# Performance work log

Measured on AMD Instinct MI355X. Metric: run time of the kernel, lower is better.

Reference implementation:

```python
import jax, jax.numpy as jnp
import numpy as np

N = 1_000_000   # total nodes
B = 20_000      # number of graphs (segments)
V = 100_000     # item vocab (rows of feat table)
D = 128         # input_dim
H = 128         # hidden_dim
O = 256         # output_dim
EPS = 1e-5


def setup_inputs() -> dict:
    key = jax.random.key(0)
    ks = jax.random.split(key, 10)
    feat = jax.random.normal(ks[0], (V, D), dtype=jnp.float32)
    iid = jax.random.randint(ks[1], (N,), 0, V)
    segment_ids = jnp.sort(jax.random.randint(ks[2], (N,), 0, B))
    last_nodes = jax.random.randint(ks[3], (B,), 0, N)
    s = 1.0 / np.sqrt(D)
    gamma = jnp.ones((D,), jnp.float32)
    beta = jnp.zeros((D,), jnp.float32)
    W_u = jax.random.uniform(ks[4], (D, H), jnp.float32, -s, s)
    W_v = jax.random.uniform(ks[5], (D, H), jnp.float32, -s, s)
    b_v = jax.random.uniform(ks[6], (H,), jnp.float32, -s, s)
    w_e = jax.random.uniform(ks[7], (H,), jnp.float32, -1.0 / np.sqrt(H), 1.0 / np.sqrt(H))
    W_out = jax.random.uniform(ks[8], (D, O), jnp.float32, -s, s)
    return {"feat": feat, "iid": iid, "segment_ids": segment_ids,
            "last_nodes": last_nodes, "gamma": gamma, "beta": beta,
            "W_u": W_u, "W_v": W_v, "b_v": b_v, "w_e": w_e, "W_out": W_out}


def reference(feat, iid, segment_ids, last_nodes, gamma, beta, W_u, W_v, b_v, w_e, W_out):
    # gather per-node features from item table
    x = feat[iid]                                  # [N, D]
    # BatchNorm1d (training mode: batch statistics, biased var)
    mean = jnp.mean(x, axis=0)
    var = jnp.mean((x - mean) ** 2, axis=0)
    x = (x - mean) * jax.lax.rsqrt(var + EPS) * gamma + beta
    # projections
    feat_u = x @ W_u                               # [N, H]
    feat_v = x[last_nodes] @ W_v + b_v             # [B, H]
    e = jax.nn.sigmoid(feat_u + feat_v[segment_ids]) @ w_e   # [N]
    # segment softmax over per-graph node segments
    e_max = jax.ops.segment_max(e, segment_ids, num_segments=B)
    ex = jnp.exp(e - e_max[segment_ids])
    denom = jax.ops.segment_sum(ex, segment_ids, num_segments=B)
    alpha = ex / denom[segment_ids]                # [N]
    # weighted segment sum, then output projection
    rst = jax.ops.segment_sum(x * alpha[:, None], segment_ids, num_segments=B)  # [B, D]
    return rst @ W_out                             # [B, O]
```

## Files before the change

### kernel.cpp

```cpp
#include <hip/hip_runtime.h>

typedef __attribute__((ext_vector_type(8))) short short8;
typedef __attribute__((ext_vector_type(4))) float floatx4;
typedef __attribute__((ext_vector_type(4))) int intx4;

static __device__ __forceinline__ unsigned short f2bf(float x) {
    unsigned int u = __float_as_uint(x);
    u += 0x7fffu + ((u >> 16) & 1u);
    return (unsigned short)(u >> 16);
}

template <int CTRL>
static __device__ __forceinline__ float dpp_add(float x) {
    int v = __builtin_amdgcn_update_dpp(0, __float_as_int(x), CTRL, 0xf, 0xf, true);
    return x + __int_as_float(v);
}

__global__ void k_hist(const int* __restrict__ iid, int* __restrict__ counts, int N) {
    int n = blockIdx.x * blockDim.x + threadIdx.x;
    if (n < N) atomicAdd(&counts[iid[n]], 1);
}

__global__ __launch_bounds__(256) void k_cvtstats(const float* __restrict__ feat,
                                                  const int* __restrict__ counts,
                                                  unsigned short* __restrict__ featb,
                                                  float* __restrict__ dsum, float* __restrict__ dsumsq,
                                                  int V) {
    int tid = threadIdx.x;
    int r2 = tid >> 7, d = tid & 127;
    float s = 0.f, qa = 0.f;
    for (int vp = blockIdx.x; vp * 2 < V; vp += gridDim.x) {
        int v = vp * 2 + r2;
        if (v >= V) continue;
        float f = feat[(size_t)v * 128 + d];
        featb[(size_t)v * 128 + d] = f2bf(f);
        float c = (float)counts[v];
        if (c != 0.f) { s += c * f; qa += c * f * f; }
    }
    __shared__ float red[256];
    red[tid] = s; __syncthreads();
    if (tid < 128) atomicAdd(&dsum[d], red[tid] + red[tid + 128]);
    __syncthreads();
    red[tid] = qa; __syncthreads();
    if (tid < 128) atomicAdd(&dsumsq[d], red[tid] + red[tid + 128]);
}

__global__ __launch_bounds__(128) void k_affine(const float* __restrict__ sum,
                                                const float* __restrict__ sumsq,
                                                const float* __restrict__ gamma,
                                                const float* __restrict__ beta,
                                                float* __restrict__ scale, float* __restrict__ shift,
                                                float invN) {
    int d = threadIdx.x;
    float mean = sum[d] * invN;
    float var  = sumsq[d] * invN - mean * mean;
    float sc   = gamma[d] * rsqrtf(var + 1e-5f);
    scale[d] = sc;
    shift[d] = beta[d] - mean * sc;
}

__global__ __launch_bounds__(128) void k_prep(const float* __restrict__ Wu, const float* __restrict__ Wv,
                                              const float* __restrict__ bv,
                                              const float* __restrict__ scale, const float* __restrict__ shift,
                                              unsigned short* __restrict__ wut, float* __restrict__ wvs,
                                              float* __restrict__ cbias) {
    int h = blockIdx.x, d = threadIdx.x;
    float sc = scale[d], sh = shift[d];
    float wu = Wu[d * 128 + h], wv = Wv[d * 128 + h];
    wut[h * 128 + d] = f2bf(sc * wu);
    wvs[d * 128 + h] = sc * wv;
    __shared__ float red[128];
    red[d] = sh * (wu + wv);
    __syncthreads();
    for (int off = 64; off > 0; off >>= 1) {
        if (d < off) red[d] += red[d + off];
        __syncthreads();
    }
    if (d == 0) cbias[h] = bv[h] + red[0];
}

__global__ __launch_bounds__(128) void k_fv(const float* __restrict__ feat, const int* __restrict__ iid,
                                            const int* __restrict__ last, const float* __restrict__ wvs,
                                            const float* __restrict__ cbias, float* __restrict__ fv,
                                            int B) {
    const int GPB = 8;
    int b0 = blockIdx.x * GPB;
    int h = threadIdx.x;
    __shared__ float sx[GPB][128];
    for (int g = 0; g < GPB; ++g) {
        int b = b0 + g;
        if (b < B) {
            int row = iid[last[b]];
            sx[g][h] = feat[(size_t)row * 128 + h];
        }
    }
    __syncthreads();
    float acc[GPB];
#pragma unroll
    for (int g = 0; g < GPB; ++g) acc[g] = 0.f;
    for (int d = 0; d < 128; ++d) {
        float w = wvs[d * 128 + h];
#pragma unroll
        for (int g = 0; g < GPB; ++g) acc[g] += sx[g][d] * w;
    }
    float c = cbias[h];
    for (int g = 0; g < GPB; ++g)
        if (b0 + g < B) fv[(size_t)(b0 + g) * 128 + h] = acc[g] + c;
}

__global__ __launch_bounds__(256, 4) void k_main(
        const unsigned short* __restrict__ featb, const int* __restrict__ iid,
        const int* __restrict__ seg, const unsigned short* __restrict__ wut,
        const float* __restrict__ fv, const float* __restrict__ we_g,
        float* __restrict__ rstAcc, float* __restrict__ den,
        int N, int B, int numTiles) {
    __shared__ unsigned short sA[2][64 * 128];
    __shared__ int   sSeg[2][64];
    __shared__ float sFv[2][4][128];
    __shared__ float sEp[4][64];

    int tid = threadIdx.x;
    int wv = tid >> 6, lane = tid & 63, q = lane >> 4, c = lane & 15;
    int p2 = lane & 15;

    short8 bfr[2][4];
    float we2[2];
#pragma unroll
    for (int t = 0; t < 2; ++t) {
        int h = (2 * wv + t) * 16 + c;
        we2[t] = we_g[h];
#pragma unroll
        for (int kc = 0; kc < 4; ++kc)
            bfr[t][kc] = *(const short8*)(wut + h * 128 + kc * 32 + q * 8);
    }

    if (blockIdx.x >= numTiles) return;

    int iidR[4]; int segR; float2 fvR;
    int rowbase = wv * 16 + (lane >> 4);
    auto loadRegs = [&](int T) {
        int n0 = T << 6;
#pragma unroll
        for (int k = 0; k < 4; ++k)
            iidR[k] = iid[min(n0 + rowbase + 4 * k, N - 1)];
        segR = seg[min(n0 + (tid & 63), N - 1)];
        int s0 = seg[min(n0, N - 1)];
        int fvrow = min(s0 + (tid >> 6), B - 1);
        fvR = *(const float2*)(fv + (size_t)fvrow * 128 + ((tid << 1) & 127));
    };
    auto stage = [&](int buf) {
        unsigned short* sAb = &sA[buf][0];
#pragma unroll
        for (int k = 0; k < 4; ++k) {
            int row = rowbase + 4 * k;
            int j = (p2 & 8) | ((p2 & 7) ^ (row & 7));
            const unsigned short* g = featb + (size_t)iidR[k] * 128 + j * 8;
            __builtin_amdgcn_global_load_lds(
                (const __attribute__((address_space(1))) void*)g,
                (__attribute__((address_space(3))) void*)(sAb + wv * 2048 + k * 512),
                16, 0, 0);
        }
        if (tid < 64) sSeg[buf][tid] = segR;
        *(float2*)&sFv[buf][tid >> 6][(tid << 1) & 127] = fvR;
    };

    int T = blockIdx.x;
    loadRegs(T);
    stage(0);
    int cur = 0;

    for (;;) {
        int Tn = T + gridDim.x;
        bool hn = (Tn < numTiles);
        if (hn) loadRegs(Tn);
        __syncthreads();
        if (hn) stage(cur ^ 1);

        floatx4 acc[4][2];
#pragma unroll
        for (int mt = 0; mt < 4; ++mt)
#pragma unroll
            for (int t = 0; t < 2; ++t) acc[mt][t] = (floatx4)(0.f);
#pragma unroll
        for (int kc = 0; kc < 4; ++kc) {
            int jj = 4 * kc + q;
            int pofs = ((jj & 8) | ((jj & 7) ^ (c & 7))) * 8;
            short8 a0 = *(const short8*)&sA[cur][( 0 + c) * 128 + pofs];
            short8 a1 = *(const short8*)&sA[cur][(16 + c) * 128 + pofs];
            short8 a2 = *(const short8*)&sA[cur][(32 + c) * 128 + pofs];
            short8 a3 = *(const short8*)&sA[cur][(48 + c) * 128 + pofs];
#pragma unroll
            for (int t = 0; t < 2; ++t) {
                acc[0][t] = __builtin_amdgcn_mfma_f32_16x16x32_bf16(a0, bfr[t][kc], acc[0][t], 0, 0, 0);
                acc[1][t] = __builtin_amdgcn_mfma_f32_16x16x32_bf16(a1, bfr[t][kc], acc[1][t], 0, 0, 0);
                acc[2][t] = __builtin_amdgcn_mfma_f32_16x16x32_bf16(a2, bfr[t][kc], acc[2][t], 0, 0, 0);
                acc[3][t] = __builtin_amdgcn_mfma_f32_16x16x32_bf16(a3, bfr[t][kc], acc[3][t], 0, 0, 0);
            }
        }
        {
            int s0 = sSeg[cur][0];
            int h0 = wv * 32 + c;
#pragma unroll
            for (int mt = 0; mt < 4; ++mt)
#pragma unroll
                for (int r = 0; r < 4; ++r) {
                    int nl = mt * 16 + q * 4 + r;
                    int sg = sSeg[cur][nl];
                    int off = sg - s0;
                    float f0, f1;
                    if (off < 4) {
                        f0 = sFv[cur][off][h0];
                        f1 = sFv[cur][off][h0 + 16];
                    } else {
                        f0 = fv[((size_t)sg << 7) + h0];
                        f1 = fv[((size_t)sg << 7) + h0 + 16];
                    }
                    float u0 = acc[mt][0][r] + f0;
                    float u1 = acc[mt][1][r] + f1;
                    float p = we2[0] * __builtin_amdgcn_rcpf(1.f + __expf(-u0))
                            + we2[1] * __builtin_amdgcn_rcpf(1.f + __expf(-u1));
                    p = dpp_add<0xb1>(p);
                    p = dpp_add<0x4e>(p);
                    p = dpp_add<0x141>(p);
                    p = dpp_add<0x140>(p);
                    if (c == 0) sEp[wv][nl] = p;
                }
        }
        asm volatile("s_waitcnt lgkmcnt(0)" ::: "memory");
        __builtin_amdgcn_s_barrier();
        __builtin_amdgcn_sched_barrier(0);

        {
            int n0 = T << 6;
            int nb = wv * 16;
            float exr[16];
#pragma unroll
            for (int jg = 0; jg < 4; ++jg) {
                floatx4 e0 = *(const floatx4*)&sEp[0][nb + jg * 4];
                floatx4 e1 = *(const floatx4*)&sEp[1][nb + jg * 4];
                floatx4 e2 = *(const floatx4*)&sEp[2][nb + jg * 4];
                floatx4 e3 = *(const floatx4*)&sEp[3][nb + jg * 4];
#pragma unroll
                for (int r = 0; r < 4; ++r) {
                    float s = e0[r] + e1[r] + e2[r] + e3[r];
                    exr[jg * 4 + r] = (n0 + nb + jg * 4 + r < N) ? __expf(s) : 0.f;
                }
            }
            int sgr[16];
#pragma unroll
            for (int jg = 0; jg < 4; ++jg)
                *(intx4*)&sgr[jg * 4] = *(const intx4*)&sSeg[cur][nb + jg * 4];

            int d0 = lane * 2;
            int jj = lane >> 2;
            int wsub = (lane & 3) * 4;
            const char* base = (const char*)&sA[cur][0];
            float a0 = 0.f, a1 = 0.f, dl = 0.f;
            int curseg = sgr[0];
#pragma unroll
            for (int j = 0; j < 16; ++j) {
                int row = nb + j;
                int sg = sgr[j];
                if (sg != curseg) {
                    atomicAdd(&rstAcc[(size_t)curseg * 128 + d0], a0);
                    atomicAdd(&rstAcc[(size_t)curseg * 128 + d0 + 1], a1);
                    if (lane == 0) atomicAdd(&den[curseg], dl);
                    a0 = a1 = dl = 0.f; curseg = sg;
                }
                int ch = (jj & 8) | ((jj & 7) ^ (row & 7));
                unsigned u = *(const unsigned*)(base + row * 256 + ch * 16 + wsub);
                float e = exr[j];
                a0 += e * __uint_as_float(u << 16);
                a1 += e * __uint_as_float(u & 0xffff0000u);
                dl += e;
            }
            atomicAdd(&rstAcc[(size_t)curseg * 128 + d0], a0);
            atomicAdd(&rstAcc[(size_t)curseg * 128 + d0 + 1], a1);
            if (lane == 0) atomicAdd(&den[curseg], dl);
        }

        if (!hn) break;
        T = Tn; cur ^= 1;
    }
}

__global__ __launch_bounds__(256) void k_out(const float* __restrict__ rstAcc,
                                             const float* __restrict__ den,
                                             const float* __restrict__ scale,
                                             const float* __restrict__ shift,
                                             const float* __restrict__ Wout,
                                             float* __restrict__ out, int B) {
    __shared__ float sT[128][36];
    __shared__ float sInv[32];
    int b0 = blockIdx.x * 32;
    int t = threadIdx.x;
    for (int i = 0; i < 16; ++i) {
        int idx = i * 256 + t;
        int r = idx >> 7, d = idx & 127;
        int b = min(b0 + r, B - 1);
        sT[d][r] = scale[d] * rstAcc[((size_t)b << 7) + d];
    }
    if (t < 32) {
        int b = min(b0 + t, B - 1);
        float dn = den[b];
        sInv[t] = (dn > 0.f) ? 1.f / dn : 0.f;
    }
    __syncthreads();
    float acc[32];
#pragma unroll
    for (int r = 0; r < 32; ++r) acc[r] = 0.f;
    float sb = 0.f;
    for (int dd = 0; dd < 128; ++dd) {
        float w = Wout[dd * 256 + t];
        sb += shift[dd] * w;
        const float4* row = (const float4*)&sT[dd][0];
#pragma unroll
        for (int r4 = 0; r4 < 8; ++r4) {
            float4 v = row[r4];
            acc[r4 * 4 + 0] += w * v.x;
            acc[r4 * 4 + 1] += w * v.y;
            acc[r4 * 4 + 2] += w * v.z;
            acc[r4 * 4 + 3] += w * v.w;
        }
    }
    for (int r = 0; r < 32; ++r)
        if (b0 + r < B) {
            float inv = sInv[r];
            out[(size_t)(b0 + r) * 256 + t] = acc[r] * inv + (inv != 0.f ? sb : 0.f);
        }
}

extern "C" void kernel_launch(void* const* d_in, const int* in_sizes, int n_in,
                              void* d_out, int out_size, void* d_ws, size_t ws_size,
                              hipStream_t stream) {
    const float* feat  = (const float*)d_in[0];
    const int*   iid   = (const int*)d_in[1];
    const int*   seg   = (const int*)d_in[2];
    const int*   last  = (const int*)d_in[3];
    const float* gamma = (const float*)d_in[4];
    const float* beta  = (const float*)d_in[5];
    const float* Wu    = (const float*)d_in[6];
    const float* Wv    = (const float*)d_in[7];
    const float* bv    = (const float*)d_in[8];
    const float* we    = (const float*)d_in[9];
    const float* Wout  = (const float*)d_in[10];
    float* out = (float*)d_out;

    int V = in_sizes[0] / 128;
    int N = in_sizes[1];
    int B = in_sizes[3];

    char* w = (char*)d_ws;
    size_t off = 0;
    auto alloc = [&](size_t bytes) -> void* {
        void* p = w + off;
        off += (bytes + 255) & ~(size_t)255;
        return p;
    };
    int*   counts = (int*)alloc((size_t)V * 4);
    float* dsum   = (float*)alloc(512);
    float* dsumsq = (float*)alloc(512);
    float* rstAcc = (float*)alloc((size_t)B * 128 * 4);
    float* den    = (float*)alloc((size_t)B * 4);
    size_t zero_bytes = off;
    float* scale  = (float*)alloc(512);
    float* shift  = (float*)alloc(512);
    float* cbias  = (float*)alloc(512);
    unsigned short* wut = (unsigned short*)alloc(128 * 128 * 2);
    float* wvs    = (float*)alloc(128 * 128 * 4);
    float* fv     = (float*)alloc((size_t)B * 128 * 4);
    unsigned short* featb = (unsigned short*)alloc((size_t)V * 128 * 2);
    (void)ws_size; (void)n_in; (void)out_size;

    hipMemsetAsync(d_ws, 0, zero_bytes, stream);

    k_hist<<<(N + 255) / 256, 256, 0, stream>>>(iid, counts, N);
    k_cvtstats<<<1024, 256, 0, stream>>>(feat, counts, featb, dsum, dsumsq, V);
    k_affine<<<1, 128, 0, stream>>>(dsum, dsumsq, gamma, beta, scale, shift, 1.0f / (float)N);
    k_prep<<<128, 128, 0, stream>>>(Wu, Wv, bv, scale, shift, wut, wvs, cbias);
    k_fv<<<(B + 7) / 8, 128, 0, stream>>>(feat, iid, last, wvs, cbias, fv, B);

    int numTiles = (N + 63) / 64;
    k_main<<<1024, 256, 0, stream>>>(featb, iid, seg, wut, fv, we, rstAcc, den, N, B, numTiles);

    k_out<<<(B + 31) / 32, 256, 0, stream>>>(rstAcc, den, scale, shift, Wout, out, B);
}
```

Baseline: 416.3 us.

## Merge all stages into one cooperative persistent kernel with grid syncs

Replaces the memset and seven separate kernel launches with one cooperative kernel that runs each stage in sequence, separated by grid-wide barriers. Zeroing is done in-kernel and the small stages (affine, prep, fv, output projection) become grid-stride loops inside the same grid. The aim is to remove launch gaps and per-kernel ramp-up and tail costs. In exchange, the small serial stages run inside a 1024-block grid where most blocks sit idle at barriers, grid.sync adds its own overhead, and occupancy is now capped by the shared-memory and register use of the largest stage.

New measurement: 960.1 us. 2.31x slower.

```diff
diff --git a/kernel.cpp b/kernel.cpp
--- a/kernel.cpp
+++ b/kernel.cpp
@@ -1,4 +1,7 @@
 #include <hip/hip_runtime.h>
+#include <hip/hip_cooperative_groups.h>
+
+namespace cg = cooperative_groups;
 
 typedef __attribute__((ext_vector_type(8))) short short8;
 typedef __attribute__((ext_vector_type(4))) float floatx4;
@@ -16,335 +19,347 @@
     return x + __int_as_float(v);
 }
 
-__global__ void k_hist(const int* __restrict__ iid, int* __restrict__ counts, int N) {
-    int n = blockIdx.x * blockDim.x + threadIdx.x;
-    if (n < N) atomicAdd(&counts[iid[n]], 1);
-}
-
-__global__ __launch_bounds__(256) void k_cvtstats(const float* __restrict__ feat,
-                                                  const int* __restrict__ counts,
-                                                  unsigned short* __restrict__ featb,
-                                                  float* __restrict__ dsum, float* __restrict__ dsumsq,
-                                                  int V) {
+struct MonoP {
+    const float* feat; const int* iid; const int* seg; const int* last;
+    const float* gamma; const float* beta; const float* Wu; const float* Wv;
+    const float* bv; const float* we; const float* Wout;
+    float* out;
+    int* counts; float* dsum; float* dsumsq; float* rstAcc; float* den;
+    float* scale; float* shift; float* cbias;
+    unsigned short* wut; float* wvs; float* fv;
+    unsigned short* featb;
+    float* zeroBase; int zeroQuads;
+    int N, B, V, numTiles;
+};
+
+__global__ __launch_bounds__(256, 4) void k_mono(MonoP p) {
+    cg::grid_group grid = cg::this_grid();
+    __shared__ __align__(16) char smem[38912];
     int tid = threadIdx.x;
-    int r2 = tid >> 7, d = tid & 127;
-    float s = 0.f, qa = 0.f;
-    for (int vp = blockIdx.x; vp * 2 < V; vp += gridDim.x) {
-        int v = vp * 2 + r2;
-        if (v >= V) continue;
-        float f = feat[(size_t)v * 128 + d];
-        featb[(size_t)v * 128 + d] = f2bf(f);
-        float c = (float)counts[v];
-        if (c != 0.f) { s += c * f; qa += c * f * f; }
-    }
-    __shared__ float red[256];
-    red[tid] = s; __syncthreads();
-    if (tid < 128) atomicAdd(&dsum[d], red[tid] + red[tid + 128]);
-    __syncthreads();
-    red[tid] = qa; __syncthreads();
-    if (tid < 128) atomicAdd(&dsumsq[d], red[tid] + red[tid + 128]);
-}
-
-__global__ __launch_bounds__(128) void k_affine(const float* __restrict__ sum,
-                                                const float* __restrict__ sumsq,
-                                                const float* __restrict__ gamma,
-                                                const float* __restrict__ beta,
-                                                float* __restrict__ scale, float* __restrict__ shift,
-                                                float invN) {
-    int d = threadIdx.x;
-    float mean = sum[d] * invN;
-    float var  = sumsq[d] * invN - mean * mean;
-    float sc   = gamma[d] * rsqrtf(var + 1e-5f);
-    scale[d] = sc;
-    shift[d] = beta[d] - mean * sc;
-}
-
-__global__ __launch_bounds__(128) void k_prep(const float* __restrict__ Wu, const float* __restrict__ Wv,
-                                              const float* __restrict__ bv,
-                                              const float* __restrict__ scale, const float* __restrict__ shift,
-                                              unsigned short* __restrict__ wut, float* __restrict__ wvs,
-                                              float* __restrict__ cbias) {
-    int h = blockIdx.x, d = threadIdx.x;
-    float sc = scale[d], sh = shift[d];
-    float wu = Wu[d * 128 + h], wv = Wv[d * 128 + h];
-    wut[h * 128 + d] = f2bf(sc * wu);
-    wvs[d * 128 + h] = sc * wv;
-    __shared__ float red[128];
-    red[d] = sh * (wu + wv);
-    __syncthreads();
-    for (int off = 64; off > 0; off >>= 1) {
-        if (d < off) red[d] += red[d + off];
+    int gtid = blockIdx.x * 256 + tid;
+    int gsz = gridDim.x * 256;
+
+    {
+        floatx4* z = (floatx4*)p.zeroBase;
+        floatx4 zz = (floatx4)(0.f);
+        for (int i = gtid; i < p.zeroQuads; i += gsz) z[i] = zz;
+    }
+    grid.sync();
+
+    for (int n = gtid; n < p.N; n += gsz) atomicAdd(&p.counts[p.iid[n]], 1);
+    grid.sync();
+
+    {
+        float* red = (float*)smem;
+        int r2 = tid >> 7, d = tid & 127;
+        float s = 0.f, qa = 0.f;
+        for (int vp = blockIdx.x; vp * 2 < p.V; vp += gridDim.x) {
+            int v = vp * 2 + r2;
+            if (v >= p.V) continue;
+            float f = p.feat[(size_t)v * 128 + d];
+            p.featb[(size_t)v * 128 + d] = f2bf(f);
+            float c = (float)p.counts[v];
+            if (c != 0.f) { s += c * f; qa += c * f * f; }
+        }
+        red[tid] = s; __syncthreads();
+        if (tid < 128) atomicAdd(&p.dsum[d], red[tid] + red[tid + 128]);
         __syncthreads();
-    }
-    if (d == 0) cbias[h] = bv[h] + red[0];
-}
-
-__global__ __launch_bounds__(128) void k_fv(const float* __restrict__ feat, const int* __restrict__ iid,
-                                            const int* __restrict__ last, const float* __restrict__ wvs,
-                                            const float* __restrict__ cbias, float* __restrict__ fv,
-                                            int B) {
-    const int GPB = 8;
-    int b0 = blockIdx.x * GPB;
-    int h = threadIdx.x;
-    __shared__ float sx[GPB][128];
-    for (int g = 0; g < GPB; ++g) {
-        int b = b0 + g;
-        if (b < B) {
-            int row = iid[last[b]];
-            sx[g][h] = feat[(size_t)row * 128 + h];
-        }
-    }
-    __syncthreads();
-    float acc[GPB];
-#pragma unroll
-    for (int g = 0; g < GPB; ++g) acc[g] = 0.f;
-    for (int d = 0; d < 128; ++d) {
-        float w = wvs[d * 128 + h];
-#pragma unroll
-        for (int g = 0; g < GPB; ++g) acc[g] += sx[g][d] * w;
-    }
-    float c = cbias[h];
-    for (int g = 0; g < GPB; ++g)
-        if (b0 + g < B) fv[(size_t)(b0 + g) * 128 + h] = acc[g] + c;
-}
-
-__global__ __launch_bounds__(256, 4) void k_main(
-        const unsigned short* __restrict__ featb, const int* __restrict__ iid,
-        const int* __restrict__ seg, const unsigned short* __restrict__ wut,
-        const float* __restrict__ fv, const float* __restrict__ we_g,
-        float* __restrict__ rstAcc, float* __restrict__ den,
-        int N, int B, int numTiles) {
-    __shared__ unsigned short sA[2][64 * 128];
-    __shared__ int   sSeg[2][64];
-    __shared__ float sFv[2][4][128];
-    __shared__ float sEp[4][64];
-
-    int tid = threadIdx.x;
-    int wv = tid >> 6, lane = tid & 63, q = lane >> 4, c = lane & 15;
-    int p2 = lane & 15;
-
-    short8 bfr[2][4];
-    float we2[2];
-#pragma unroll
-    for (int t = 0; t < 2; ++t) {
-        int h = (2 * wv + t) * 16 + c;
-        we2[t] = we_g[h];
-#pragma unroll
-        for (int kc = 0; kc < 4; ++kc)
-            bfr[t][kc] = *(const short8*)(wut + h * 128 + kc * 32 + q * 8);
-    }
-
-    if (blockIdx.x >= numTiles) return;
-
-    int iidR[4]; int segR; float2 fvR;
-    int rowbase = wv * 16 + (lane >> 4);
-    auto loadRegs = [&](int T) {
-        int n0 = T << 6;
-#pragma unroll
-        for (int k = 0; k < 4; ++k)
-            iidR[k] = iid[min(n0 + rowbase + 4 * k, N - 1)];
-        segR = seg[min(n0 + (tid & 63), N - 1)];
-        int s0 = seg[min(n0, N - 1)];
-        int fvrow = min(s0 + (tid >> 6), B - 1);
-        fvR = *(const float2*)(fv + (size_t)fvrow * 128 + ((tid << 1) & 127));
-    };
-    auto stage = [&](int buf) {
-        unsigned short* sAb = &sA[buf][0];
-#pragma unroll
-        for (int k = 0; k < 4; ++k) {
-            int row = rowbase + 4 * k;
-            int j = (p2 & 8) | ((p2 & 7) ^ (row & 7));
-            const unsigned short* g = featb + (size_t)iidR[k] * 128 + j * 8;
-            __builtin_amdgcn_global_load_lds(
-                (const __attribute__((address_space(1))) void*)g,
-                (__attribute__((address_space(3))) void*)(sAb + wv * 2048 + k * 512),
-                16, 0, 0);
-        }
-        if (tid < 64) sSeg[buf][tid] = segR;
-        *(float2*)&sFv[buf][tid >> 6][(tid << 1) & 127] = fvR;
-    };
-
-    int T = blockIdx.x;
-    loadRegs(T);
-    stage(0);
-    int cur = 0;
-
-    for (;;) {
-        int Tn = T + gridDim.x;
-        bool hn = (Tn < numTiles);
-        if (hn) loadRegs(Tn);
+        red[tid] = qa; __syncthreads();
+        if (tid < 128) atomicAdd(&p.dsumsq[d], red[tid] + red[tid + 128]);
+    }
+    grid.sync();
+
+    if (blockIdx.x == 0 && tid < 128) {
+        int d = tid;
+        float invN = 1.f / (float)p.N;
+        float mean = p.dsum[d] * invN;
+        float var  = p.dsumsq[d] * invN - mean * mean;
+        float sc   = p.gamma[d] * rsqrtf(var + 1e-5f);
+        p.scale[d] = sc;
+        p.shift[d] = p.beta[d] - mean * sc;
+    }
+    grid.sync();
+
+    if (blockIdx.x < 64) {
+        float (*red)[128] = (float(*)[128])smem;
+        int d = tid & 127, half = tid >> 7;
+        int h = blockIdx.x * 2 + half;
+        float sc = p.scale[d], sh = p.shift[d];
+        float wu = p.Wu[d * 128 + h], wvv = p.Wv[d * 128 + h];
+        p.wut[h * 128 + d] = f2bf(sc * wu);
+        p.wvs[d * 128 + h] = sc * wvv;
+        red[half][d] = sh * (wu + wvv);
         __syncthreads();
-        if (hn) stage(cur ^ 1);
-
-        floatx4 acc[4][2];
-#pragma unroll
-        for (int mt = 0; mt < 4; ++mt)
-#pragma unroll
-            for (int t = 0; t < 2; ++t) acc[mt][t] = (floatx4)(0.f);
-#pragma unroll
-        for (int kc = 0; kc < 4; ++kc) {
-            int jj = 4 * kc + q;
-            int pofs = ((jj & 8) | ((jj & 7) ^ (c & 7))) * 8;
-            short8 a0 = *(const short8*)&sA[cur][( 0 + c) * 128 + pofs];
-            short8 a1 = *(const short8*)&sA[cur][(16 + c) * 128 + pofs];
-            short8 a2 = *(const short8*)&sA[cur][(32 + c) * 128 + pofs];
-            short8 a3 = *(const short8*)&sA[cur][(48 + c) * 128 + pofs];
-#pragma unroll
-            for (int t = 0; t < 2; ++t) {
-                acc[0][t] = __builtin_amdgcn_mfma_f32_16x16x32_bf16(a0, bfr[t][kc], acc[0][t], 0, 0, 0);
-                acc[1][t] = __builtin_amdgcn_mfma_f32_16x16x32_bf16(a1, bfr[t][kc], acc[1][t], 0, 0, 0);
-                acc[2][t] = __builtin_amdgcn_mfma_f32_16x16x32_bf16(a2, bfr[t][kc], acc[2][t], 0, 0, 0);
-                acc[3][t] = __builtin_amdgcn_mfma_f32_16x16x32_bf16(a3, bfr[t][kc], acc[3][t], 0, 0, 0);
-            }
-        }
-        {
-            int s0 = sSeg[cur][0];
-            int h0 = wv * 32 + c;
+        for (int off = 64; off > 0; off >>= 1) {
+            if (d < off) red[half][d] += red[half][d + off];
+            __syncthreads();
+        }
+        if (d == 0) p.cbias[h] = p.bv[h] + red[half][0];
+    }
+    grid.sync();
+
+    {
+        float (*sx)[128] = (float(*)[128])smem;
+        int h = tid & 127, half = tid >> 7;
+        int njob = (p.B + 15) >> 4;
+        for (int job = blockIdx.x; job < njob; job += gridDim.x) {
+            __syncthreads();
+            for (int g = 0; g < 8; ++g) {
+                int b = job * 16 + half * 8 + g;
+                if (b < p.B) {
+                    int row = p.iid[p.last[b]];
+                    sx[half * 8 + g][h] = p.feat[(size_t)row * 128 + h];
+                }
+            }
+            __syncthreads();
+            float acc[8];
+#pragma unroll
+            for (int g = 0; g < 8; ++g) acc[g] = 0.f;
+            for (int d = 0; d < 128; ++d) {
+                float w = p.wvs[d * 128 + h];
+#pragma unroll
+                for (int g = 0; g < 8; ++g) acc[g] += sx[half * 8 + g][d] * w;
+            }
+            float cb = p.cbias[h];
+            for (int g = 0; g < 8; ++g) {
+                int b = job * 16 + half * 8 + g;
+                if (b < p.B) p.fv[(size_t)b * 128 + h] = acc[g] + cb;
+            }
+        }
+    }
+    grid.sync();
+
+    if (blockIdx.x < p.numTiles) {
+        auto sA   = (unsigned short(*)[64 * 128])(smem);
+        auto sSeg = (int(*)[64])(smem + 32768);
+        auto sFv  = (float(*)[4][128])(smem + 33280);
+        auto sEp  = (float(*)[64])(smem + 37376);
+
+        int wv = tid >> 6, lane = tid & 63, q = lane >> 4, c = lane & 15;
+        int p2 = lane & 15;
+
+        short8 bfr[2][4];
+        float we2[2];
+#pragma unroll
+        for (int t = 0; t < 2; ++t) {
+            int h = (2 * wv + t) * 16 + c;
+            we2[t] = p.we[h];
+#pragma unroll
+            for (int kc = 0; kc < 4; ++kc)
+                bfr[t][kc] = *(const short8*)(p.wut + h * 128 + kc * 32 + q * 8);
+        }
+
+        int iidR[4]; int segR; float2 fvR;
+        int rowbase = wv * 16 + (lane >> 4);
+        auto loadRegs = [&](int T) {
+            int n0 = T << 6;
+#pragma unroll
+            for (int k = 0; k < 4; ++k)
+                iidR[k] = p.iid[min(n0 + rowbase + 4 * k, p.N - 1)];
+            segR = p.seg[min(n0 + (tid & 63), p.N - 1)];
+            int s0 = p.seg[min(n0, p.N - 1)];
+            int fvrow = min(s0 + (tid >> 6), p.B - 1);
+            fvR = *(const float2*)(p.fv + (size_t)fvrow * 128 + ((tid << 1) & 127));
+        };
+        auto stage = [&](int buf) {
+            unsigned short* sAb = &sA[buf][0];
+#pragma unroll
+            for (int k = 0; k < 4; ++k) {
+                int row = rowbase + 4 * k;
+                int j = (p2 & 8) | ((p2 & 7) ^ (row & 7));
+                const unsigned short* g = p.featb + (size_t)iidR[k] * 128 + j * 8;
+                __builtin_amdgcn_global_load_lds(
+                    (const __attribute__((address_space(1))) void*)g,
+                    (__attribute__((address_space(3))) void*)(sAb + wv * 2048 + k * 512),
+                    16, 0, 0);
+            }
+            if (tid < 64) sSeg[buf][tid] = segR;
+            *(float2*)&sFv[buf][tid >> 6][(tid << 1) & 127] = fvR;
+        };
+
+        int T = blockIdx.x;
+        loadRegs(T);
+        stage(0);
+        int cur = 0;
+
+        for (;;) {
+            int Tn = T + gridDim.x;
+            bool hn = (Tn < p.numTiles);
+            if (hn) loadRegs(Tn);
+            __syncthreads();
+            if (hn) stage(cur ^ 1);
+
+            floatx4 acc[4][2];
 #pragma unroll
             for (int mt = 0; mt < 4; ++mt)
 #pragma unroll
-                for (int r = 0; r < 4; ++r) {
-                    int nl = mt * 16 + q * 4 + r;
-                    int sg = sSeg[cur][nl];
-                    int off = sg - s0;
-                    float f0, f1;
-                    if (off < 4) {
-                        f0 = sFv[cur][off][h0];
-                        f1 = sFv[cur][off][h0 + 16];
-                    } else {
-                        f0 = fv[((size_t)sg << 7) + h0];
-                        f1 = fv[((size_t)sg << 7) + h0 + 16];
+                for (int t = 0; t < 2; ++t) acc[mt][t] = (floatx4)(0.f);
+#pragma unroll
+            for (int kc = 0; kc < 4; ++kc) {
+                int jj = 4 * kc + q;
+                int pofs = ((jj & 8) | ((jj & 7) ^ (c & 7))) * 8;
+                short8 a0 = *(const short8*)&sA[cur][( 0 + c) * 128 + pofs];
+                short8 a1 = *(const short8*)&sA[cur][(16 + c) * 128 + pofs];
+                short8 a2 = *(const short8*)&sA[cur][(32 + c) * 128 + pofs];
+                short8 a3 = *(const short8*)&sA[cur][(48 + c) * 128 + pofs];
+#pragma unroll
+                for (int t = 0; t < 2; ++t) {
+                    acc[0][t] = __builtin_amdgcn_mfma_f32_16x16x32_bf16(a0, bfr[t][kc], acc[0][t], 0, 0, 0);
+                    acc[1][t] = __builtin_amdgcn_mfma_f32_16x16x32_bf16(a1, bfr[t][kc], acc[1][t], 0, 0, 0);
+                    acc[2][t] = __builtin_amdgcn_mfma_f32_16x16x32_bf16(a2, bfr[t][kc], acc[2][t], 0, 0, 0);
+                    acc[3][t] = __builtin_amdgcn_mfma_f32_16x16x32_bf16(a3, bfr[t][kc], acc[3][t], 0, 0, 0);
+                }
+            }
+            {
+                int s0 = sSeg[cur][0];
+                int h0 = wv * 32 + c;
+#pragma unroll
+                for (int mt = 0; mt < 4; ++mt)
+#pragma unroll
+                    for (int r = 0; r < 4; ++r) {
+                        int nl = mt * 16 + q * 4 + r;
+                        int sg = sSeg[cur][nl];
+                        int off = sg - s0;
+                        float f0, f1;
+                        if (off < 4) {
+                            f0 = sFv[cur][off][h0];
+                            f1 = sFv[cur][off][h0 + 16];
+                        } else {
+                            f0 = p.fv[((size_t)sg << 7) + h0];
+                            f1 = p.fv[((size_t)sg << 7) + h0 + 16];
+                        }
+                        float u0 = acc[mt][0][r] + f0;
+                        float u1 = acc[mt][1][r] + f1;
+                        float pp = we2[0] * __builtin_amdgcn_rcpf(1.f + __expf(-u0))
+                                 + we2[1] * __builtin_amdgcn_rcpf(1.f + __expf(-u1));
+                        pp = dpp_add<0xb1>(pp);
+                        pp = dpp_add<0x4e>(pp);
+                        pp = dpp_add<0x141>(pp);
+                        pp = dpp_add<0x140>(pp);
+                        if (c == 0) sEp[wv][nl] = pp;
                     }
-                    float u0 = acc[mt][0][r] + f0;
-                    float u1 = acc[mt][1][r] + f1;
-                    float p = we2[0] * __builtin_amdgcn_rcpf(1.f + __expf(-u0))
-                            + we2[1] * __builtin_amdgcn_rcpf(1.f + __expf(-u1));
-                    p = dpp_add<0xb1>(p);
-                    p = dpp_add<0x4e>(p);
-                    p = dpp_add<0x141>(p);
-                    p = dpp_add<0x140>(p);
-                    if (c == 0) sEp[wv][nl] = p;
-                }
-        }
-        asm volatile("s_waitcnt lgkmcnt(0)" ::: "memory");
-        __builtin_amdgcn_s_barrier();
-        __builtin_amdgcn_sched_barrier(0);
-
-        {
-            int n0 = T << 6;
-            int nb = wv * 16;
-            float exr[16];
-#pragma unroll
-            for (int jg = 0; jg < 4; ++jg) {
-                floatx4 e0 = *(const floatx4*)&sEp[0][nb + jg * 4];
-                floatx4 e1 = *(const floatx4*)&sEp[1][nb + jg * 4];
-                floatx4 e2 = *(const floatx4*)&sEp[2][nb + jg * 4];
-                floatx4 e3 = *(const floatx4*)&sEp[3][nb + jg * 4];
-#pragma unroll
-                for (int r = 0; r < 4; ++r) {
-                    float s = e0[r] + e1[r] + e2[r] + e3[r];
-                    exr[jg * 4 + r] = (n0 + nb + jg * 4 + r < N) ? __expf(s) : 0.f;
-                }
-            }
-            int sgr[16];
-#pragma unroll
-            for (int jg = 0; jg < 4; ++jg)
-                *(intx4*)&sgr[jg * 4] = *(const intx4*)&sSeg[cur][nb + jg * 4];
-
-            int d0 = lane * 2;
-            int jj = lane >> 2;
-            int wsub = (lane & 3) * 4;
-            const char* base = (const char*)&sA[cur][0];
-            float a0 = 0.f, a1 = 0.f, dl = 0.f;
-            int curseg = sgr[0];
-#pragma unroll
-            for (int j = 0; j < 16; ++j) {
-                int row = nb + j;
-                int sg = sgr[j];
-                if (sg != curseg) {
-                    atomicAdd(&rstAcc[(size_t)curseg * 128 + d0], a0);
-                    atomicAdd(&rstAcc[(size_t)curseg * 128 + d0 + 1], a1);
-                    if (lane == 0) atomicAdd(&den[curseg], dl);
-                    a0 = a1 = dl = 0.f; curseg = sg;
-                }
-                int ch = (jj & 8) | ((jj & 7) ^ (row & 7));
-                unsigned u = *(const unsigned*)(base + row * 256 + ch * 16 + wsub);
-                float e = exr[j];
-                a0 += e * __uint_as_float(u << 16);
-                a1 += e * __uint_as_float(u & 0xffff0000u);
-                dl += e;
-            }
-            atomicAdd(&rstAcc[(size_t)curseg * 128 + d0], a0);
-            atomicAdd(&rstAcc[(size_t)curseg * 128 + d0 + 1], a1);
-            if (lane == 0) atomicAdd(&den[curseg], dl);
-        }
-
-        if (!hn) break;
-        T = Tn; cur ^= 1;
-    }
-}
-
-__global__ __launch_bounds__(256) void k_out(const float* __restrict__ rstAcc,
-                                             const float* __restrict__ den,
-                                             const float* __restrict__ scale,
-                                             const float* __restrict__ shift,
-                                             const float* __restrict__ Wout,
-                                             float* __restrict__ out, int B) {
-    __shared__ float sT[128][36];
-    __shared__ float sInv[32];
-    int b0 = blockIdx.x * 32;
-    int t = threadIdx.x;
-    for (int i = 0; i < 16; ++i) {
-        int idx = i * 256 + t;
-        int r = idx >> 7, d = idx & 127;
-        int b = min(b0 + r, B - 1);
-        sT[d][r] = scale[d] * rstAcc[((size_t)b << 7) + d];
-    }
-    if (t < 32) {
-        int b = min(b0 + t, B - 1);
-        float dn = den[b];
-        sInv[t] = (dn > 0.f) ? 1.f / dn : 0.f;
-    }
-    __syncthreads();
-    float acc[32];
-#pragma unroll
-    for (int r = 0; r < 32; ++r) acc[r] = 0.f;
-    float sb = 0.f;
-    for (int dd = 0; dd < 128; ++dd) {
-        float w = Wout[dd * 256 + t];
-        sb += shift[dd] * w;
-        const float4* row = (const float4*)&sT[dd][0];
-#pragma unroll
-        for (int r4 = 0; r4 < 8; ++r4) {
-            float4 v = row[r4];
-            acc[r4 * 4 + 0] += w * v.x;
-            acc[r4 * 4 + 1] += w * v.y;
-            acc[r4 * 4 + 2] += w * v.z;
-            acc[r4 * 4 + 3] += w * v.w;
-        }
-    }
-    for (int r = 0; r < 32; ++r)
-        if (b0 + r < B) {
-            float inv = sInv[r];
-            out[(size_t)(b0 + r) * 256 + t] = acc[r] * inv + (inv != 0.f ? sb : 0.f);
-        }
+            }
+            asm volatile("s_waitcnt lgkmcnt(0)" ::: "memory");
+            __builtin_amdgcn_s_barrier();
+            __builtin_amdgcn_sched_barrier(0);
+
+            {
+                int n0 = T << 6;
+                int nb = wv * 16;
+                float exr[16];
+#pragma unroll
+                for (int jg = 0; jg < 4; ++jg) {
+                    floatx4 e0 = *(const floatx4*)&sEp[0][nb + jg * 4];
+                    floatx4 e1 = *(const floatx4*)&sEp[1][nb + jg * 4];
+                    floatx4 e2 = *(const floatx4*)&sEp[2][nb + jg * 4];
+                    floatx4 e3 = *(const floatx4*)&sEp[3][nb + jg * 4];
+#pragma unroll
+                    for (int r = 0; r < 4; ++r) {
+                        float s = e0[r] + e1[r] + e2[r] + e3[r];
+                        exr[jg * 4 + r] = (n0 + nb + jg * 4 + r < p.N) ? __expf(s) : 0.f;
+                    }
+                }
+                int sgr[16];
+#pragma unroll
+                for (int jg = 0; jg < 4; ++jg)
+                    *(intx4*)&sgr[jg * 4] = *(const intx4*)&sSeg[cur][nb + jg * 4];
+
+                int d0 = lane * 2;
+                int jj = lane >> 2;
+                int wsub = (lane & 3) * 4;
+                const char* base = (const char*)&sA[cur][0];
+                float a0 = 0.f, a1 = 0.f, dl = 0.f;
+                int curseg = sgr[0];
+#pragma unroll
+                for (int j = 0; j < 16; ++j) {
+                    int row = nb + j;
+                    int sg = sgr[j];
+                    if (sg != curseg) {
+                        atomicAdd(&p.rstAcc[(size_t)curseg * 128 + d0], a0);
+                        atomicAdd(&p.rstAcc[(size_t)curseg * 128 + d0 + 1], a1);
+                        if (lane == 0) atomicAdd(&p.den[curseg], dl);
+                        a0 = a1 = dl = 0.f; curseg = sg;
+                    }
+                    int ch = (jj & 8) | ((jj & 7) ^ (row & 7));
+                    unsigned u = *(const unsigned*)(base + row * 256 + ch * 16 + wsub);
+                    float e = exr[j];
+                    a0 += e * __uint_as_float(u << 16);
+                    a1 += e * __uint_as_float(u & 0xffff0000u);
+                    dl += e;
+                }
+                atomicAdd(&p.rstAcc[(size_t)curseg * 128 + d0], a0);
+                atomicAdd(&p.rstAcc[(size_t)curseg * 128 + d0 + 1], a1);
+                if (lane == 0) atomicAdd(&p.den[curseg], dl);
+            }
+
+            if (!hn) break;
+            T = Tn; cur ^= 1;
+        }
+    }
+    grid.sync();
+
+    {
+        float (*sT)[36] = (float(*)[36])smem;
+        float* sInv = (float*)(smem + 18432);
+        int njob = (p.B + 31) >> 5;
+        for (int job = blockIdx.x; job < njob; job += gridDim.x) {
+            __syncthreads();
+            int b0 = job * 32;
+            int t = tid;
+            for (int i = 0; i < 16; ++i) {
+                int idx = i * 256 + t;
+                int r = idx >> 7, d = idx & 127;
+                int b = min(b0 + r, p.B - 1);
+                sT[d][r] = p.scale[d] * p.rstAcc[((size_t)b << 7) + d];
+            }
+            if (t < 32) {
+                int b = min(b0 + t, p.B - 1);
+                float dn = p.den[b];
+                sInv[t] = (dn > 0.f) ? 1.f / dn : 0.f;
+            }
+            __syncthreads();
+            float acc[32];
+#pragma unroll
+            for (int r = 0; r < 32; ++r) acc[r] = 0.f;
+            float sb = 0.f;
+            for (int dd = 0; dd < 128; ++dd) {
+                float w = p.Wout[dd * 256 + t];
+                sb += p.shift[dd] * w;
+                const float4* row = (const float4*)&sT[dd][0];
+#pragma unroll
+                for (int r4 = 0; r4 < 8; ++r4) {
+                    float4 v = row[r4];
+                    acc[r4 * 4 + 0] += w * v.x;
+                    acc[r4 * 4 + 1] += w * v.y;
+                    acc[r4 * 4 + 2] += w * v.z;
+                    acc[r4 * 4 + 3] += w * v.w;
+                }
+            }
+            for (int r = 0; r < 32; ++r)
+                if (b0 + r < p.B) {
+                    float inv = sInv[r];
+                    p.out[(size_t)(b0 + r) * 256 + t] = acc[r] * inv + (inv != 0.f ? sb : 0.f);
+                }
+        }
+    }
 }
 
 extern "C" void kernel_launch(void* const* d_in, const int* in_sizes, int n_in,
                               void* d_out, int out_size, void* d_ws, size_t ws_size,
                               hipStream_t stream) {
-    const float* feat  = (const float*)d_in[0];
-    const int*   iid   = (const int*)d_in[1];
-    const int*   seg   = (const int*)d_in[2];
-    const int*   last  = (const int*)d_in[3];
-    const float* gamma = (const float*)d_in[4];
-    const float* beta  = (const float*)d_in[5];
-    const float* Wu    = (const float*)d_in[6];
-    const float* Wv    = (const float*)d_in[7];
-    const float* bv    = (const float*)d_in[8];
-    const float* we    = (const float*)d_in[9];
-    const float* Wout  = (const float*)d_in[10];
-    float* out = (float*)d_out;
+    MonoP prm;
+    prm.feat  = (const float*)d_in[0];
+    prm.iid   = (const int*)d_in[1];
+    prm.seg   = (const int*)d_in[2];
+    prm.last  = (const int*)d_in[3];
+    prm.gamma = (const float*)d_in[4];
+    prm.beta  = (const float*)d_in[5];
+    prm.Wu    = (const float*)d_in[6];
+    prm.Wv    = (const float*)d_in[7];
+    prm.bv    = (const float*)d_in[8];
+    prm.we    = (const float*)d_in[9];
+    prm.Wout  = (const float*)d_in[10];
+    prm.out   = (float*)d_out;
 
     int V = in_sizes[0] / 128;
     int N = in_sizes[1];
@@ -353,35 +368,37 @@
     char* w = (char*)d_ws;
     size_t off = 0;
     auto alloc = [&](size_t bytes) -> void* {
-        void* p = w + off;
+        void* pp = w + off;
         off += (bytes + 255) & ~(size_t)255;
-        return p;
+        return pp;
     };
-    int*   counts = (int*)alloc((size_t)V * 4);
-    float* dsum   = (float*)alloc(512);
-    float* dsumsq = (float*)alloc(512);
-    float* rstAcc = (float*)alloc((size_t)B * 128 * 4);
-    float* den    = (float*)alloc((size_t)B * 4);
+    prm.counts = (int*)alloc((size_t)V * 4);
+    prm.dsum   = (float*)alloc(512);
+    prm.dsumsq = (float*)alloc(512);
+    prm.rstAcc = (float*)alloc((size_t)B * 128 * 4);
+    prm.den    = (float*)alloc((size_t)B * 4);
     size_t zero_bytes = off;
-    float* scale  = (float*)alloc(512);
-    float* shift  = (float*)alloc(512);
-    float* cbias  = (float*)alloc(512);
-    unsigned short* wut = (unsigned short*)alloc(128 * 128 * 2);
-    float* wvs    = (float*)alloc(128 * 128 * 4);
-    float* fv     = (float*)alloc((size_t)B * 128 * 4);
-    unsigned short* featb = (unsigned short*)alloc((size_t)V * 128 * 2);
+    prm.scale  = (float*)alloc(512);
+    prm.shift  = (float*)alloc(512);
+    prm.cbias  = (float*)alloc(512);
+    prm.wut    = (unsigned short*)alloc(128 * 128 * 2);
+    prm.wvs    = (float*)alloc(128 * 128 * 4);
+    prm.fv     = (float*)alloc((size_t)B * 128 * 4);
+    prm.featb  = (unsigned short*)alloc((size_t)V * 128 * 2);
     (void)ws_size; (void)n_in; (void)out_size;
 
-    hipMemsetAsync(d_ws, 0, zero_bytes, stream);
-
-    k_hist<<<(N + 255) / 256, 256, 0, stream>>>(iid, counts, N);
-    k_cvtstats<<<1024, 256, 0, stream>>>(feat, counts, featb, dsum, dsumsq, V);
-    k_affine<<<1, 128, 0, stream>>>(dsum, dsumsq, gamma, beta, scale, shift, 1.0f / (float)N);
-    k_prep<<<128, 128, 0, stream>>>(Wu, Wv, bv, scale, shift, wut, wvs, cbias);
-    k_fv<<<(B + 7) / 8, 128, 0, stream>>>(feat, iid, last, wvs, cbias, fv, B);
-
-    int numTiles = (N + 63) / 64;
-    k_main<<<1024, 256, 0, stream>>>(featb, iid, seg, wut, fv, we, rstAcc, den, N, B, numTiles);
-
-    k_out<<<(B + 31) / 32, 256, 0, stream>>>(rstAcc, den, scale, shift, Wout, out, B);
+    prm.zeroBase  = (float*)d_ws;
+    prm.zeroQuads = (int)(zero_bytes / 16);
+    prm.N = N; prm.B = B; prm.V = V;
+    prm.numTiles = (N + 63) / 64;
+
+    int maxB = 0;
+    hipOccupancyMaxActiveBlocksPerMultiprocessor(&maxB, k_mono, 256, 0);
+    if (maxB < 1) maxB = 1;
+    int grid = maxB * 256;
+    if (grid > 1024) grid = 1024;
+
+    void* args[] = { (void*)&prm };
+    hipLaunchCooperativeKernel((const void*)k_mono, dim3(grid), dim3(256),
+                               args, 0, stream);
 }
```

## Fuse affine into prep, move accumulator zeroing into k_fv, use exp2 math

Applied to the files above, without the earlier changes.

Folds the BatchNorm affine computation into k_prep, which removes one kernel launch. Zeroing of rstAcc/den moves from the memset into the k_fv kernel, so the memset only clears counts and the stats buffers. In k_main, log2(e) is folded into fv and w_e so the sigmoid and softmax exponentials use the native exp2 instead of __expf. s0 now comes from readfirstlane instead of a separate global load. This trims launch overhead and ALU work, at the cost of a scalar multiply on the uncached fv path and slightly different rounding.

Measured after the change: 490.2 us. 17.8% more time.

```diff
diff --git a/kernel.cpp b/kernel.cpp
--- a/kernel.cpp
+++ b/kernel.cpp
@@ -45,27 +45,20 @@
     if (tid < 128) atomicAdd(&dsumsq[d], red[tid] + red[tid + 128]);
 }
 
-__global__ __launch_bounds__(128) void k_affine(const float* __restrict__ sum,
-                                                const float* __restrict__ sumsq,
-                                                const float* __restrict__ gamma,
-                                                const float* __restrict__ beta,
-                                                float* __restrict__ scale, float* __restrict__ shift,
-                                                float invN) {
-    int d = threadIdx.x;
-    float mean = sum[d] * invN;
-    float var  = sumsq[d] * invN - mean * mean;
-    float sc   = gamma[d] * rsqrtf(var + 1e-5f);
-    scale[d] = sc;
-    shift[d] = beta[d] - mean * sc;
-}
-
 __global__ __launch_bounds__(128) void k_prep(const float* __restrict__ Wu, const float* __restrict__ Wv,
                                               const float* __restrict__ bv,
-                                              const float* __restrict__ scale, const float* __restrict__ shift,
+                                              const float* __restrict__ gamma, const float* __restrict__ beta,
+                                              const float* __restrict__ dsum, const float* __restrict__ dsumsq,
+                                              float invN,
                                               unsigned short* __restrict__ wut, float* __restrict__ wvs,
+                                              float* __restrict__ scale, float* __restrict__ shift,
                                               float* __restrict__ cbias) {
     int h = blockIdx.x, d = threadIdx.x;
-    float sc = scale[d], sh = shift[d];
+    float mean = dsum[d] * invN;
+    float var  = dsumsq[d] * invN - mean * mean;
+    float sc   = gamma[d] * rsqrtf(var + 1e-5f);
+    float sh   = beta[d] - mean * sc;
+    if (h == 0) { scale[d] = sc; shift[d] = sh; }
     float wu = Wu[d * 128 + h], wv = Wv[d * 128 + h];
     wut[h * 128 + d] = f2bf(sc * wu);
     wvs[d * 128 + h] = sc * wv;
@@ -82,7 +75,15 @@
 __global__ __launch_bounds__(128) void k_fv(const float* __restrict__ feat, const int* __restrict__ iid,
                                             const int* __restrict__ last, const float* __restrict__ wvs,
                                             const float* __restrict__ cbias, float* __restrict__ fv,
+                                            float* __restrict__ zeroBase, int zeroQuads,
                                             int B) {
+    {
+        int gt = blockIdx.x * 128 + threadIdx.x;
+        int gs = gridDim.x * 128;
+        floatx4 zz = (floatx4)(0.f);
+        floatx4* z = (floatx4*)zeroBase;
+        for (int i = gt; i < zeroQuads; i += gs) z[i] = zz;
+    }
     const int GPB = 8;
     int b0 = blockIdx.x * GPB;
     int h = threadIdx.x;
@@ -119,6 +120,9 @@
     __shared__ float sFv[2][4][128];
     __shared__ float sEp[4][64];
 
+    const float NL2E = -1.44269504f;
+    const float L2E  =  1.44269504f;
+
     int tid = threadIdx.x;
     int wv = tid >> 6, lane = tid & 63, q = lane >> 4, c = lane & 15;
     int p2 = lane & 15;
@@ -128,7 +132,7 @@
 #pragma unroll
     for (int t = 0; t < 2; ++t) {
         int h = (2 * wv + t) * 16 + c;
-        we2[t] = we_g[h];
+        we2[t] = we_g[h] * L2E;
 #pragma unroll
         for (int kc = 0; kc < 4; ++kc)
             bfr[t][kc] = *(const short8*)(wut + h * 128 + kc * 32 + q * 8);
@@ -144,9 +148,10 @@
         for (int k = 0; k < 4; ++k)
             iidR[k] = iid[min(n0 + rowbase + 4 * k, N - 1)];
         segR = seg[min(n0 + (tid & 63), N - 1)];
-        int s0 = seg[min(n0, N - 1)];
+        int s0 = __builtin_amdgcn_readfirstlane(segR);
         int fvrow = min(s0 + (tid >> 6), B - 1);
         fvR = *(const float2*)(fv + (size_t)fvrow * 128 + ((tid << 1) & 127));
+        fvR.x *= NL2E; fvR.y *= NL2E;
     };
     auto stage = [&](int buf) {
         unsigned short* sAb = &sA[buf][0];
@@ -212,13 +217,13 @@
                         f0 = sFv[cur][off][h0];
                         f1 = sFv[cur][off][h0 + 16];
                     } else {
-                        f0 = fv[((size_t)sg << 7) + h0];
-                        f1 = fv[((size_t)sg << 7) + h0 + 16];
+                        f0 = NL2E * fv[((size_t)sg << 7) + h0];
+                        f1 = NL2E * fv[((size_t)sg << 7) + h0 + 16];
                     }
-                    float u0 = acc[mt][0][r] + f0;
-                    float u1 = acc[mt][1][r] + f1;
-                    float p = we2[0] * __builtin_amdgcn_rcpf(1.f + __expf(-u0))
-                            + we2[1] * __builtin_amdgcn_rcpf(1.f + __expf(-u1));
+                    float m0 = __builtin_fmaf(acc[mt][0][r], NL2E, f0);
+                    float m1 = __builtin_fmaf(acc[mt][1][r], NL2E, f1);
+                    float p = we2[0] * __builtin_amdgcn_rcpf(1.f + __builtin_amdgcn_exp2f(m0))
+                            + we2[1] * __builtin_amdgcn_rcpf(1.f + __builtin_amdgcn_exp2f(m1));
                     p = dpp_add<0xb1>(p);
                     p = dpp_add<0x4e>(p);
                     p = dpp_add<0x141>(p);
@@ -243,7 +248,7 @@
 #pragma unroll
                 for (int r = 0; r < 4; ++r) {
                     float s = e0[r] + e1[r] + e2[r] + e3[r];
-                    exr[jg * 4 + r] = (n0 + nb + jg * 4 + r < N) ? __expf(s) : 0.f;
+                    exr[jg * 4 + r] = (n0 + nb + jg * 4 + r < N) ? __builtin_amdgcn_exp2f(s) : 0.f;
                 }
             }
             int sgr[16];
@@ -360,9 +365,11 @@
     int*   counts = (int*)alloc((size_t)V * 4);
     float* dsum   = (float*)alloc(512);
     float* dsumsq = (float*)alloc(512);
+    size_t memset_bytes = off;
+    size_t zstart = off;
     float* rstAcc = (float*)alloc((size_t)B * 128 * 4);
     float* den    = (float*)alloc((size_t)B * 4);
-    size_t zero_bytes = off;
+    size_t zbytes = off - zstart;
     float* scale  = (float*)alloc(512);
     float* shift  = (float*)alloc(512);
     float* cbias  = (float*)alloc(512);
@@ -372,13 +379,14 @@
     unsigned short* featb = (unsigned short*)alloc((size_t)V * 128 * 2);
     (void)ws_size; (void)n_in; (void)out_size;
 
-    hipMemsetAsync(d_ws, 0, zero_bytes, stream);
+    hipMemsetAsync(d_ws, 0, memset_bytes, stream);
 
     k_hist<<<(N + 255) / 256, 256, 0, stream>>>(iid, counts, N);
     k_cvtstats<<<1024, 256, 0, stream>>>(feat, counts, featb, dsum, dsumsq, V);
-    k_affine<<<1, 128, 0, stream>>>(dsum, dsumsq, gamma, beta, scale, shift, 1.0f / (float)N);
-    k_prep<<<128, 128, 0, stream>>>(Wu, Wv, bv, scale, shift, wut, wvs, cbias);
-    k_fv<<<(B + 7) / 8, 128, 0, stream>>>(feat, iid, last, wvs, cbias, fv, B);
+    k_prep<<<128, 128, 0, stream>>>(Wu, Wv, bv, gamma, beta, dsum, dsumsq,
+                                    1.0f / (float)N, wut, wvs, scale, shift, cbias);
+    k_fv<<<(B + 7) / 8, 128, 0, stream>>>(feat, iid, last, wvs, cbias, fv,
+                                          rstAcc, (int)(zbytes / 16), B);
 
     int numTiles = (N + 63) / 64;
     k_main<<<1024, 256, 0, stream>>>(featb, iid, seg, wut, fv, we, rstAcc, den, N, B, numTiles);
```
